# Kernel tuning notes

Measured on AMD Instinct MI355X. Metric: run time of the kernel, lower is better.

## Reference

```python
import jax, jax.numpy as jnp
import numpy as np
import math

B, S, D, H = 4, 1024, 2048, 16
DH = D // H          # dim_head = 128
DHID = 128           # dim_hid
DKER = 64            # dim_ker
EPS = 1e-6


def setup_inputs() -> dict:
    key = jax.random.key(0)
    ks = jax.random.split(key, 12)
    a1 = math.sqrt(6.0 / (DH + DHID))
    a2 = math.sqrt(6.0 / (DKER + DHID))
    a3 = math.sqrt(6.0 / (2 * DKER))
    return {
        "q": jax.random.normal(ks[0], (B, S, D), jnp.float32),
        "k": jax.random.normal(ks[1], (B, S, D), jnp.float32),
        "v": jax.random.normal(ks[2], (B, S, D), jnp.float32),
        "lr_attn_mask": jax.random.randint(ks[3], (B, 1, S, S), 0, 2).astype(bool),
        "sparse_norms_lse": jax.random.normal(ks[4], (B, H, S, 1), jnp.float32),
        "sparse_attn_weights": jax.random.normal(ks[5], (B, H, S, S), jnp.float32),
        "kernel_q_mat1": jax.random.uniform(ks[6], (H, DH, DHID), jnp.float32, -a1, a1),
        "kernel_k_mat1": jax.random.uniform(ks[7], (H, DH, DHID), jnp.float32, -a1, a1),
        "kernel_q_mat2": jax.random.uniform(ks[8], (H, DHID, DKER), jnp.float32, -a2, a2),
        "kernel_k_mat2": jax.random.uniform(ks[9], (H, DHID, DKER), jnp.float32, -a2, a2),
        "interaction_k": jax.random.uniform(ks[10], (H, DKER, DKER), jnp.float32, -a3, a3),
        "scalingD": jnp.ones((1, H, 1, DKER), jnp.float32) * 1e-4,
        "scalingD2": jnp.ones((1, H, 1, DKER), jnp.float32) * 1e-4,
        "lambda_constant": 1,
    }


def _gelu(x):
    # torch F.gelu default = exact (erf) gelu
    return jax.nn.gelu(x, approximate=False)


def reference(q, k, v, lr_attn_mask, sparse_norms_lse, sparse_attn_weights,
              kernel_q_mat1, kernel_k_mat1, kernel_q_mat2, kernel_k_mat2,
              interaction_k, scalingD, scalingD2, lambda_constant):
    # split heads: [B,S,D] -> [B,H,S,DH]
    qh = q.reshape(B, S, H, DH).transpose(0, 2, 1, 3)
    kh = k.reshape(B, S, H, DH).transpose(0, 2, 1, 3)
    vh = v.reshape(B, S, H, DH).transpose(0, 2, 1, 3)

    # learned kernel feature maps (dropout=0 -> identity)
    qf = _gelu(jnp.einsum('bhsd,hde->bhse', qh, kernel_q_mat1))
    qf = _gelu(jnp.einsum('bhse,hef->bhsf', qf, kernel_q_mat2))

    kf = _gelu(jnp.einsum('bhsd,hde->bhse', kh, kernel_k_mat1))
    kf = jnp.abs(scalingD) * _gelu(jnp.einsum('bhse,hef->bhsf', kf, kernel_k_mat2))
    kf = kf + jnp.einsum('bhse,hef->bhsf', kf, interaction_k) * scalingD2

    # low-rank (kernelized) scores, masked. [B,H,S,S]
    scores = jnp.einsum('bhse,bhte->bhst', jnp.abs(qf), jnp.abs(kf))
    m = lr_attn_mask.astype(scores.dtype)  # [B,1,S,S] broadcasts
    scores = m * scores

    # log-domain merge with external sparse attention
    lr_norms_lse = jnp.log(scores.sum(axis=-1, keepdims=True) + EPS)
    norm_factor_lse = jnp.logaddexp(lr_norms_lse, sparse_norms_lse)
    logits = jnp.log(scores + EPS) * m + (1.0 - m) * sparse_attn_weights
    attn = jnp.exp(logits - norm_factor_lse)

    out = jnp.einsum('bhst,bhtd->bhsd', attn, vh)
    return out.transpose(0, 2, 1, 3).reshape(B, S, D)
```

## Files before the change

### kernel.cpp

```cpp
#include <hip/hip_runtime.h>


typedef __bf16 bf16_t;
typedef __attribute__((ext_vector_type(8))) __bf16 bf16x8;
typedef __attribute__((ext_vector_type(4))) float f32x4;

#define MFMA(a, b, c) __builtin_amdgcn_mfma_f32_16x16x32_bf16((a), (b), (c), 0, 0, 0)

typedef __attribute__((address_space(3))) void as3_void;
typedef __attribute__((address_space(1))) const void as1_void;
static __device__ __forceinline__ void gload16(const void* g, void* l) {
    __builtin_amdgcn_global_load_lds((as1_void*)g, (as3_void*)l, 16, 0, 0);
}

static __device__ __forceinline__ float gelu_exact(float x) {
    return 0.5f * x * (1.0f + erff(x * 0.70710678118654752f));
}

__global__ __launch_bounds__(256) void conv_weights_kernel(
    const float* __restrict__ wq1, const float* __restrict__ wk1,
    const float* __restrict__ wq2, const float* __restrict__ wk2,
    const float* __restrict__ iK,
    bf16_t* __restrict__ wq1t, bf16_t* __restrict__ wk1t,
    bf16_t* __restrict__ wq2t, bf16_t* __restrict__ wk2t,
    bf16_t* __restrict__ iKt)
{
    const int idx = blockIdx.x * 256 + threadIdx.x;
    if (idx < 16 * 128 * 128) {
        int h = idx >> 14, e = (idx >> 7) & 127, d = idx & 127;
        wq1t[idx] = (bf16_t)wq1[(h << 14) + (d << 7) + e];
        wk1t[idx] = (bf16_t)wk1[(h << 14) + (d << 7) + e];
    }
    if (idx < 16 * 64 * 128) {
        int h = idx >> 13, f = (idx >> 7) & 63, e = idx & 127;
        wq2t[idx] = (bf16_t)wq2[(h << 13) + (e << 6) + f];
        wk2t[idx] = (bf16_t)wk2[(h << 13) + (e << 6) + f];
    }
    if (idx < 16 * 64 * 64) {
        int h = idx >> 12, g = (idx >> 6) & 63, f = idx & 63;
        iKt[idx] = (bf16_t)iK[(h << 12) + (f << 6) + g];
    }
}

__global__ __launch_bounds__(256) void conv_v_kernel(
    const float* __restrict__ v, bf16_t* __restrict__ vT)
{
    __shared__ bf16_t tr[128][72];
    const int bh = blockIdx.x, b = bh >> 4, h = bh & 15;
    const int tt = blockIdx.y;
    const int t0 = tt * 64;
    const int tid = threadIdx.x;
#pragma unroll
    for (int i = 0; i < 8; ++i) {
        int f4 = tid + 256 * i;
        int t = f4 >> 5, c4 = f4 & 31;
        const float4 vv = *reinterpret_cast<const float4*>(
            &v[((size_t)b * 1024 + t0 + t) * 2048 + h * 128 + c4 * 4]);
        tr[c4 * 4 + 0][t] = (bf16_t)vv.x;
        tr[c4 * 4 + 1][t] = (bf16_t)vv.y;
        tr[c4 * 4 + 2][t] = (bf16_t)vv.z;
        tr[c4 * 4 + 3][t] = (bf16_t)vv.w;
    }
    __syncthreads();
#pragma unroll
    for (int i = 0; i < 32; ++i) {
        int e = tid + 256 * i;
        int d = e >> 6, tl = e & 63;
        vT[(((size_t)bh * 16 + tt) * 128 + d) * 64 + tl] = tr[d][tl];
    }
}

__global__ __launch_bounds__(256) void feat_kernel(
    const float* __restrict__ q, const float* __restrict__ k,
    const bf16_t* __restrict__ wq1t, const bf16_t* __restrict__ wq2t,
    const bf16_t* __restrict__ wk1t, const bf16_t* __restrict__ wk2t,
    const bf16_t* __restrict__ iKt,
    const float* __restrict__ sD, const float* __restrict__ sD2,
    bf16_t* __restrict__ qf, bf16_t* __restrict__ kf)
{
    __shared__ bf16_t xa[64][136];
    __shared__ bf16_t h1[64][136];
    __shared__ bf16_t k2[64][72];

    const int tid = threadIdx.x;
    const int lane = tid & 63, w = tid >> 6;
    const int lr = lane & 15, lg = lane >> 4;
    const int row0 = blockIdx.x * 64;
    const int h = blockIdx.y;
    const int path = blockIdx.z;

    const float* X = path ? k : q;
    const bf16_t* w1t = path ? wk1t : wq1t;
    const bf16_t* w2t = path ? wk2t : wq2t;
    bf16_t* outp = path ? kf : qf;

#pragma unroll
    for (int i = 0; i < 8; ++i) {
        int f4 = tid + 256 * i;
        int r = f4 >> 5, c4 = f4 & 31;
        const float4 vv = *reinterpret_cast<const float4*>(
            &X[(size_t)(row0 + r) * 2048 + h * 128 + c4 * 4]);
        xa[r][c4 * 4 + 0] = (bf16_t)vv.x;
        xa[r][c4 * 4 + 1] = (bf16_t)vv.y;
        xa[r][c4 * 4 + 2] = (bf16_t)vv.z;
        xa[r][c4 * 4 + 3] = (bf16_t)vv.w;
    }
    __syncthreads();

    bf16x8 a1[4];
#pragma unroll
    for (int kk = 0; kk < 4; ++kk)
        a1[kk] = *reinterpret_cast<const bf16x8*>(&xa[w * 16 + lr][kk * 32 + lg * 8]);
#pragma unroll
    for (int nt = 0; nt < 8; ++nt) {
        f32x4 acc = {0.f, 0.f, 0.f, 0.f};
#pragma unroll
        for (int kk = 0; kk < 4; ++kk) {
            bf16x8 bfr = *reinterpret_cast<const bf16x8*>(
                &w1t[(size_t)h * 16384 + (nt * 16 + lr) * 128 + kk * 32 + lg * 8]);
            acc = MFMA(a1[kk], bfr, acc);
        }
#pragma unroll
        for (int r = 0; r < 4; ++r)
            h1[w * 16 + lg * 4 + r][nt * 16 + lr] = (bf16_t)gelu_exact(acc[r]);
    }
    __syncthreads();

    bf16x8 a2[4];
#pragma unroll
    for (int kk = 0; kk < 4; ++kk)
        a2[kk] = *reinterpret_cast<const bf16x8*>(&h1[w * 16 + lr][kk * 32 + lg * 8]);

    if (path == 0) {
#pragma unroll
        for (int nt = 0; nt < 4; ++nt) {
            f32x4 acc = {0.f, 0.f, 0.f, 0.f};
#pragma unroll
            for (int kk = 0; kk < 4; ++kk) {
                bf16x8 bfr = *reinterpret_cast<const bf16x8*>(
                    &w2t[(size_t)h * 8192 + (nt * 16 + lr) * 128 + kk * 32 + lg * 8]);
                acc = MFMA(a2[kk], bfr, acc);
            }
#pragma unroll
            for (int r = 0; r < 4; ++r) {
                int n = row0 + w * 16 + lg * 4 + r;
                int bb = n >> 10, s = n & 1023;
                outp[(((size_t)bb * 16 + h) * 1024 + s) * 64 + nt * 16 + lr] =
                    (bf16_t)fabsf(gelu_exact(acc[r]));
            }
        }
    } else {
#pragma unroll
        for (int nt = 0; nt < 4; ++nt) {
            f32x4 acc = {0.f, 0.f, 0.f, 0.f};
#pragma unroll
            for (int kk = 0; kk < 4; ++kk) {
                bf16x8 bfr = *reinterpret_cast<const bf16x8*>(
                    &w2t[(size_t)h * 8192 + (nt * 16 + lr) * 128 + kk * 32 + lg * 8]);
                acc = MFMA(a2[kk], bfr, acc);
            }
#pragma unroll
            for (int r = 0; r < 4; ++r) {
                int f = nt * 16 + lr;
                k2[w * 16 + lg * 4 + r][f] =
                    (bf16_t)(fabsf(sD[h * 64 + f]) * gelu_exact(acc[r]));
            }
        }
        __syncthreads();
        bf16x8 a3[2];
#pragma unroll
        for (int kk = 0; kk < 2; ++kk)
            a3[kk] = *reinterpret_cast<const bf16x8*>(&k2[w * 16 + lr][kk * 32 + lg * 8]);
#pragma unroll
        for (int nt = 0; nt < 4; ++nt) {
            f32x4 acc = {0.f, 0.f, 0.f, 0.f};
#pragma unroll
            for (int kk = 0; kk < 2; ++kk) {
                bf16x8 bfr = *reinterpret_cast<const bf16x8*>(
                    &iKt[(size_t)h * 4096 + (nt * 16 + lr) * 64 + kk * 32 + lg * 8]);
                acc = MFMA(a3[kk], bfr, acc);
            }
#pragma unroll
            for (int r = 0; r < 4; ++r) {
                int row = w * 16 + lg * 4 + r;
                int g = nt * 16 + lr;
                float base = (float)k2[row][g];
                float kv = fabsf(base + acc[r] * sD2[h * 64 + g]);
                int n = row0 + row;
                int bb = n >> 10, s = n & 1023;
                outp[(((size_t)bb * 16 + h) * 1024 + s) * 64 + g] = (bf16_t)kv;
            }
        }
    }
}

__global__ __launch_bounds__(256, 2) void attn_fused_kernel(
    const bf16_t* __restrict__ qf, const bf16_t* __restrict__ kf,
    const bf16_t* __restrict__ vT,
    const unsigned char* __restrict__ mask8,
    const float* __restrict__ saw, const float* __restrict__ lse,
    float* __restrict__ out)
{
    __shared__ bf16_t vbuf[2][128 * 64];
    __shared__ bf16_t ebuf[2][64 * 72];
    __shared__ int mflag;

    const int tid = threadIdx.x;
    const int lane = tid & 63, w = tid >> 6;
    const int lr = lane & 15, lg = lane >> 4;

    const int di = blockIdx.y * 16 + blockIdx.x;
    const int xcd = di & 7, rr = di >> 3;
    const int bh = xcd + 8 * (rr >> 4);
    const int s0 = (rr & 15) * 64;
    const int b = bh >> 4, h = bh & 15;

    if (tid == 0) {
        unsigned a = 0;
        for (int i = 0; i < 64; ++i) a |= mask8[4 * i + 1];
        mflag = (a == 0) ? 1 : 0;
    }
    __syncthreads();
    const bool mask_is_int = (mflag != 0);
    const int* mask32 = (const int*)mask8;

    const int strow = tid >> 4;
    const int stcol = (tid & 15) * 4;
    const size_t saw_base = ((size_t)bh << 20) + (size_t)(s0 + strow) * 1024 + stcol;
    const size_t m_base   = ((size_t)b << 20) + (size_t)(s0 + strow) * 1024 + stcol;

    const int vrow = tid >> 3;
    const int vcol8 = (tid & 7) ^ (vrow & 7);
    const bf16_t* vt_bh = vT + (size_t)bh * 131072;

    bf16x8 aq0, aq1;
    {
        const size_t qb = ((size_t)bh * 1024 + s0 + w * 16 + lr) * 64;
        aq0 = *reinterpret_cast<const bf16x8*>(&qf[qb + lg * 8]);
        aq1 = *reinterpret_cast<const bf16x8*>(&qf[qb + 32 + lg * 8]);
    }

    const f32x4 fzero = {0.f, 0.f, 0.f, 0.f};
    f32x4 oacc[8];
#pragma unroll
    for (int i = 0; i < 8; ++i) oacc[i] = fzero;
    float rowsum[4] = {0.f, 0.f, 0.f, 0.f};

#define STAGE_VT(BUF, TILE)                                                      \
    {                                                                            \
        const bf16_t* vg = vt_bh + (size_t)(TILE) * 8192 + vcol8 * 8;            \
        char* lb = (char*)&vbuf[BUF][0] + w * 1024;                              \
        _Pragma("unroll")                                                        \
        for (int j = 0; j < 4; ++j)                                              \
            gload16(vg + (size_t)(32 * j + vrow) * 64, lb + j * 4096);           \
    }

#define LOAD_KF(TILE, KR)                                                        \
    {                                                                            \
        _Pragma("unroll")                                                        \
        for (int nt = 0; nt < 4; ++nt) {                                         \
            const size_t kb = ((size_t)bh * 1024 + (TILE) * 64 + nt * 16 + lr) * 64; \
            KR[nt * 2]     = *reinterpret_cast<const bf16x8*>(&kf[kb + lg * 8]); \
            KR[nt * 2 + 1] = *reinterpret_cast<const bf16x8*>(&kf[kb + 32 + lg * 8]); \
        }                                                                        \
    }

#define LOAD_SAWM(TILE, SS, MI, MU)                                              \
    {                                                                            \
        _Pragma("unroll")                                                        \
        for (int j = 0; j < 4; ++j)                                              \
            SS[j] = *reinterpret_cast<const float4*>(                            \
                &saw[saw_base + (size_t)(TILE) * 64 + (size_t)j * 16384]);       \
        if (mask_is_int) {                                                       \
            _Pragma("unroll")                                                    \
            for (int j = 0; j < 4; ++j)                                          \
                MI[j] = *reinterpret_cast<const int4*>(                          \
                    &mask32[m_base + (size_t)(TILE) * 64 + (size_t)j * 16384]);  \
        } else {                                                                 \
            _Pragma("unroll")                                                    \
            for (int j = 0; j < 4; ++j)                                          \
                MU[j] = *reinterpret_cast<const unsigned*>(                      \
                    &mask8[m_base + (size_t)(TILE) * 64 + (size_t)j * 16384]);   \
        }                                                                        \
    }

#define WRITE_EBUF(BUF, SS, MI, MU)                                              \
    {                                                                            \
        _Pragma("unroll")                                                        \
        for (int j = 0; j < 4; ++j) {                                            \
            int m0, m1, m2, m3;                                                  \
            if (mask_is_int) {                                                   \
                m0 = MI[j].x; m1 = MI[j].y; m2 = MI[j].z; m3 = MI[j].w;          \
            } else {                                                             \
                m0 = (int)(MU[j] & 255u);        m1 = (int)((MU[j] >> 8) & 255u);\
                m2 = (int)((MU[j] >> 16) & 255u); m3 = (int)(MU[j] >> 24);       \
            }                                                                    \
            bf16_t e[4];                                                         \
            e[0] = m0 ? (bf16_t)(-1.0f) : (bf16_t)__expf(SS[j].x);               \
            e[1] = m1 ? (bf16_t)(-1.0f) : (bf16_t)__expf(SS[j].y);               \
            e[2] = m2 ? (bf16_t)(-1.0f) : (bf16_t)__expf(SS[j].z);               \
            e[3] = m3 ? (bf16_t)(-1.0f) : (bf16_t)__expf(SS[j].w);               \
            *reinterpret_cast<uint2*>(&ebuf[BUF][(strow + 16 * j) * 72 + stcol]) \
                = *reinterpret_cast<const uint2*>(e);                            \
        }                                                                        \
    }

#define PHASE(CUR, KR)                                                           \
    {                                                                            \
        f32x4 c[4];                                                              \
        _Pragma("unroll")                                                        \
        for (int nt = 0; nt < 4; ++nt) {                                         \
            f32x4 acc = fzero;                                                   \
            acc = MFMA(aq0, KR[nt * 2], acc);                                    \
            acc = MFMA(aq1, KR[nt * 2 + 1], acc);                                \
            c[nt] = acc;                                                         \
        }                                                                        \
        _Pragma("unroll")                                                        \
        for (int nt = 0; nt < 4; ++nt) {                                         \
            _Pragma("unroll")                                                    \
            for (int r = 0; r < 4; ++r) {                                        \
                const int eoff = (w * 16 + lg * 4 + r) * 72 + nt * 16 + lr;      \
                float pe = (float)ebuf[CUR][eoff];                               \
                float sc = c[nt][r];                                             \
                bool msk = pe < 0.f;                                             \
                float wv = msk ? (sc + 1e-6f) : pe;                              \
                rowsum[r] += msk ? sc : 0.f;                                     \
                ebuf[CUR][eoff] = (bf16_t)wv;                                    \
            }                                                                    \
        }                                                                        \
        asm volatile("s_waitcnt lgkmcnt(0)" ::: "memory");                       \
        __builtin_amdgcn_sched_barrier(0);                                       \
        bf16x8 ap0 = *reinterpret_cast<const bf16x8*>(                           \
            &ebuf[CUR][(w * 16 + lr) * 72 + lg * 8]);                            \
        bf16x8 ap1 = *reinterpret_cast<const bf16x8*>(                           \
            &ebuf[CUR][(w * 16 + lr) * 72 + 32 + lg * 8]);                       \
        const char* vb = (const char*)&vbuf[CUR][0];                             \
        _Pragma("unroll")                                                        \
        for (int dt = 0; dt < 8; ++dt) {                                         \
            const int row = dt * 16 + lr;                                        \
            bf16x8 v0 = *reinterpret_cast<const bf16x8*>(                        \
                vb + row * 128 + ((lg * 16) ^ xorv));                            \
            bf16x8 v1 = *reinterpret_cast<const bf16x8*>(                        \
                vb + row * 128 + ((64 + lg * 16) ^ xorv));                       \
            oacc[dt] = MFMA(ap0, v0, oacc[dt]);                                  \
            oacc[dt] = MFMA(ap1, v1, oacc[dt]);                                  \
        }                                                                        \
    }

    float4 sawA[4], sawB[4];
    int4 miA[4], miB[4];
    unsigned muA[4], muB[4];
    bf16x8 kfA[8], kfB[8];
    const int xorv = (lr & 7) << 4;

    LOAD_SAWM(0, sawA, miA, muA);
    WRITE_EBUF(0, sawA, miA, muA);
    LOAD_SAWM(1, sawA, miA, muA);
    LOAD_KF(0, kfA);
    STAGE_VT(0, 0);
    __syncthreads();

    for (int i = 0; i < 16; i += 2) {
        STAGE_VT(1, i + 1);
        LOAD_KF(i + 1, kfB);
        LOAD_SAWM((i + 2) & 15, sawB, miB, muB);
        PHASE(0, kfA);
        WRITE_EBUF(1, sawA, miA, muA);
        __syncthreads();
        STAGE_VT(0, (i + 2) & 15);
        LOAD_KF((i + 2) & 15, kfA);
        LOAD_SAWM((i + 3) & 15, sawA, miA, muA);
        PHASE(1, kfB);
        WRITE_EBUF(0, sawB, miB, muB);
        __syncthreads();
    }

#pragma unroll
    for (int r = 0; r < 4; ++r) {
        float s = rowsum[r];
#pragma unroll
        for (int m = 1; m < 16; m <<= 1) s += __shfl_xor(s, m);
        rowsum[r] = s;
    }
    float invden[4];
#pragma unroll
    for (int r = 0; r < 4; ++r) {
        const int srow = s0 + w * 16 + lg * 4 + r;
        invden[r] = 1.0f / (rowsum[r] + 1e-6f + __expf(lse[(size_t)bh * 1024 + srow]));
    }
#pragma unroll
    for (int dt = 0; dt < 8; ++dt) {
#pragma unroll
        for (int r = 0; r < 4; ++r) {
            const int srow = s0 + w * 16 + lg * 4 + r;
            out[((size_t)b * 1024 + srow) * 2048 + h * 128 + dt * 16 + lr] =
                oacc[dt][r] * invden[r];
        }
    }
#undef STAGE_VT
#undef LOAD_KF
#undef LOAD_SAWM
#undef WRITE_EBUF
#undef PHASE
}

extern "C" void kernel_launch(void* const* d_in, const int* in_sizes, int n_in,
                              void* d_out, int out_size, void* d_ws, size_t ws_size,
                              hipStream_t stream)
{
    const float* q   = (const float*)d_in[0];
    const float* k   = (const float*)d_in[1];
    const float* v   = (const float*)d_in[2];
    const unsigned char* mask = (const unsigned char*)d_in[3];
    const float* lse = (const float*)d_in[4];
    const float* saw = (const float*)d_in[5];
    const float* wq1 = (const float*)d_in[6];
    const float* wk1 = (const float*)d_in[7];
    const float* wq2 = (const float*)d_in[8];
    const float* wk2 = (const float*)d_in[9];
    const float* iK  = (const float*)d_in[10];
    const float* sD  = (const float*)d_in[11];
    const float* sD2 = (const float*)d_in[12];
    float* out = (float*)d_out;

    bf16_t* wsb  = (bf16_t*)d_ws;
    bf16_t* wq1t = wsb;
    bf16_t* wk1t = wq1t + 262144;
    bf16_t* wq2t = wk1t + 262144;
    bf16_t* wk2t = wq2t + 131072;
    bf16_t* iKt  = wk2t + 131072;
    bf16_t* qf   = iKt  + 65536;
    bf16_t* kf   = qf   + 4194304;
    bf16_t* vT   = kf   + 4194304;

    conv_weights_kernel<<<dim3(1024), dim3(256), 0, stream>>>(
        wq1, wk1, wq2, wk2, iK, wq1t, wk1t, wq2t, wk2t, iKt);
    conv_v_kernel<<<dim3(64, 16), dim3(256), 0, stream>>>(v, vT);
    feat_kernel<<<dim3(64, 16, 2), dim3(256), 0, stream>>>(
        q, k, wq1t, wq2t, wk1t, wk2t, iKt, sD, sD2, qf, kf);
    attn_fused_kernel<<<dim3(16, 64), dim3(256), 0, stream>>>(
        qf, kf, vT, mask, saw, lse, out);
}
```

Before: 212.1 us.

## Swap MFMA operand order in attention and pre-normalize mask into byte buffer

```diff
diff --git a/kernel.cpp b/kernel.cpp
--- a/kernel.cpp
+++ b/kernel.cpp
@@ -15,6 +15,13 @@
 
 static __device__ __forceinline__ float gelu_exact(float x) {
     return 0.5f * x * (1.0f + erff(x * 0.70710678118654752f));
+}
+
+static __device__ __forceinline__ unsigned pack_bf16(float a, float b) {
+    bf16_t x = (bf16_t)a, y = (bf16_t)b;
+    unsigned short ux = __builtin_bit_cast(unsigned short, x);
+    unsigned short uy = __builtin_bit_cast(unsigned short, y);
+    return (unsigned)ux | ((unsigned)uy << 16);
 }
 
 __global__ __launch_bounds__(256) void conv_weights_kernel(
@@ -39,6 +46,47 @@
     if (idx < 16 * 64 * 64) {
         int h = idx >> 12, g = (idx >> 6) & 63, f = idx & 63;
         iKt[idx] = (bf16_t)iK[(h << 12) + (f << 6) + g];
+    }
+}
+
+__global__ __launch_bounds__(256) void prep_mask_kernel(
+    const unsigned char* __restrict__ mask8, unsigned char* __restrict__ mout)
+{
+    __shared__ int mflag;
+    const int tid = threadIdx.x;
+    if (tid == 0) {
+        unsigned a = 0;
+        for (int i = 0; i < 64; ++i) a |= mask8[4 * i + 1];
+        mflag = (a == 0) ? 1 : 0;
+    }
+    __syncthreads();
+    const size_t base = ((size_t)blockIdx.x * 256 + tid) * 16;
+    if (mflag) {
+        const int* mi = (const int*)mask8;
+        uint4 r;
+        unsigned bs[4];
+#pragma unroll
+        for (int j = 0; j < 4; ++j) {
+            int4 v = *reinterpret_cast<const int4*>(&mi[base + j * 4]);
+            bs[j] = (v.x ? 1u : 0u) | ((v.y ? 1u : 0u) << 8) |
+                    ((v.z ? 1u : 0u) << 16) | ((v.w ? 1u : 0u) << 24);
+        }
+        r.x = bs[0]; r.y = bs[1]; r.z = bs[2]; r.w = bs[3];
+        *reinterpret_cast<uint4*>(&mout[base]) = r;
+    } else {
+        uint4 v = *reinterpret_cast<const uint4*>(&mask8[base]);
+        uint4 r;
+        unsigned* pv = (unsigned*)&v;
+        unsigned* pr = (unsigned*)&r;
+#pragma unroll
+        for (int j = 0; j < 4; ++j) {
+            unsigned x = pv[j], o = 0;
+#pragma unroll
+            for (int k = 0; k < 4; ++k)
+                o |= (((x >> (8 * k)) & 255u) ? 1u : 0u) << (8 * k);
+            pr[j] = o;
+        }
+        *reinterpret_cast<uint4*>(&mout[base]) = r;
     }
 }
 
@@ -194,16 +242,15 @@
     }
 }
 
-__global__ __launch_bounds__(256, 2) void attn_fused_kernel(
+__global__ __launch_bounds__(256, 3) void attn_swapped_kernel(
     const bf16_t* __restrict__ qf, const bf16_t* __restrict__ kf,
     const bf16_t* __restrict__ vT,
-    const unsigned char* __restrict__ mask8,
+    const unsigned char* __restrict__ mprep,
     const float* __restrict__ saw, const float* __restrict__ lse,
     float* __restrict__ out)
 {
     __shared__ bf16_t vbuf[2][128 * 64];
-    __shared__ bf16_t ebuf[2][64 * 72];
-    __shared__ int mflag;
+    __shared__ unsigned p_lds[4][16][36];
 
     const int tid = threadIdx.x;
     const int lane = tid & 63, w = tid >> 6;
@@ -215,19 +262,9 @@
     const int s0 = (rr & 15) * 64;
     const int b = bh >> 4, h = bh & 15;
 
-    if (tid == 0) {
-        unsigned a = 0;
-        for (int i = 0; i < 64; ++i) a |= mask8[4 * i + 1];
-        mflag = (a == 0) ? 1 : 0;
-    }
-    __syncthreads();
-    const bool mask_is_int = (mflag != 0);
-    const int* mask32 = (const int*)mask8;
-
-    const int strow = tid >> 4;
-    const int stcol = (tid & 15) * 4;
-    const size_t saw_base = ((size_t)bh << 20) + (size_t)(s0 + strow) * 1024 + stcol;
-    const size_t m_base   = ((size_t)b << 20) + (size_t)(s0 + strow) * 1024 + stcol;
+    const int srow = s0 + w * 16 + lr;
+    const size_t saw_row = ((size_t)bh << 20) + (size_t)srow * 1024;
+    const size_t m_row   = ((size_t)b << 20) + (size_t)srow * 1024;
 
     const int vrow = tid >> 3;
     const int vcol8 = (tid & 7) ^ (vrow & 7);
@@ -235,7 +272,7 @@
 
     bf16x8 aq0, aq1;
     {
-        const size_t qb = ((size_t)bh * 1024 + s0 + w * 16 + lr) * 64;
+        const size_t qb = ((size_t)bh * 1024 + srow) * 64;
         aq0 = *reinterpret_cast<const bf16x8*>(&qf[qb + lg * 8]);
         aq1 = *reinterpret_cast<const bf16x8*>(&qf[qb + 32 + lg * 8]);
     }
@@ -244,7 +281,8 @@
     f32x4 oacc[8];
 #pragma unroll
     for (int i = 0; i < 8; ++i) oacc[i] = fzero;
-    float rowsum[4] = {0.f, 0.f, 0.f, 0.f};
+    float rowsum = 0.f;
+    const int xorv = (lr & 7) << 4;
 
 #define STAGE_VT(BUF, TILE)                                                      \
     {                                                                            \
@@ -255,6 +293,17 @@
             gload16(vg + (size_t)(32 * j + vrow) * 64, lb + j * 4096);           \
     }
 
+#define LOAD_SAW(TILE, SS, MM)                                                   \
+    {                                                                            \
+        _Pragma("unroll")                                                        \
+        for (int nt = 0; nt < 4; ++nt) {                                         \
+            SS[nt] = *reinterpret_cast<const f32x4*>(                            \
+                &saw[saw_row + (TILE) * 64 + nt * 16 + lg * 4]);                 \
+            MM[nt] = *reinterpret_cast<const unsigned*>(                         \
+                &mprep[m_row + (TILE) * 64 + nt * 16 + lg * 4]);                 \
+        }                                                                        \
+    }
+
 #define LOAD_KF(TILE, KR)                                                        \
     {                                                                            \
         _Pragma("unroll")                                                        \
@@ -265,75 +314,55 @@
         }                                                                        \
     }
 
-#define LOAD_SAWM(TILE, SS, MI, MU)                                              \
-    {                                                                            \
-        _Pragma("unroll")                                                        \
-        for (int j = 0; j < 4; ++j)                                              \
-            SS[j] = *reinterpret_cast<const float4*>(                            \
-                &saw[saw_base + (size_t)(TILE) * 64 + (size_t)j * 16384]);       \
-        if (mask_is_int) {                                                       \
-            _Pragma("unroll")                                                    \
-            for (int j = 0; j < 4; ++j)                                          \
-                MI[j] = *reinterpret_cast<const int4*>(                          \
-                    &mask32[m_base + (size_t)(TILE) * 64 + (size_t)j * 16384]);  \
-        } else {                                                                 \
-            _Pragma("unroll")                                                    \
-            for (int j = 0; j < 4; ++j)                                          \
-                MU[j] = *reinterpret_cast<const unsigned*>(                      \
-                    &mask8[m_base + (size_t)(TILE) * 64 + (size_t)j * 16384]);   \
-        }                                                                        \
-    }
-
-#define WRITE_EBUF(BUF, SS, MI, MU)                                              \
-    {                                                                            \
-        _Pragma("unroll")                                                        \
-        for (int j = 0; j < 4; ++j) {                                            \
-            int m0, m1, m2, m3;                                                  \
-            if (mask_is_int) {                                                   \
-                m0 = MI[j].x; m1 = MI[j].y; m2 = MI[j].z; m3 = MI[j].w;          \
-            } else {                                                             \
-                m0 = (int)(MU[j] & 255u);        m1 = (int)((MU[j] >> 8) & 255u);\
-                m2 = (int)((MU[j] >> 16) & 255u); m3 = (int)(MU[j] >> 24);       \
-            }                                                                    \
-            bf16_t e[4];                                                         \
-            e[0] = m0 ? (bf16_t)(-1.0f) : (bf16_t)__expf(SS[j].x);               \
-            e[1] = m1 ? (bf16_t)(-1.0f) : (bf16_t)__expf(SS[j].y);               \
-            e[2] = m2 ? (bf16_t)(-1.0f) : (bf16_t)__expf(SS[j].z);               \
-            e[3] = m3 ? (bf16_t)(-1.0f) : (bf16_t)__expf(SS[j].w);               \
-            *reinterpret_cast<uint2*>(&ebuf[BUF][(strow + 16 * j) * 72 + stcol]) \
-                = *reinterpret_cast<const uint2*>(e);                            \
-        }                                                                        \
-    }
-
-#define PHASE(CUR, KR)                                                           \
+#define PHASE(CUR, SS, MM)                                                       \
     {                                                                            \
         f32x4 c[4];                                                              \
         _Pragma("unroll")                                                        \
         for (int nt = 0; nt < 4; ++nt) {                                         \
             f32x4 acc = fzero;                                                   \
-            acc = MFMA(aq0, KR[nt * 2], acc);                                    \
-            acc = MFMA(aq1, KR[nt * 2 + 1], acc);                                \
+            acc = MFMA(kfR[nt * 2], aq0, acc);                                   \
+            acc = MFMA(kfR[nt * 2 + 1], aq1, acc);                               \
             c[nt] = acc;                                                         \
         }                                                                        \
+        unsigned pk[8];                                                          \
         _Pragma("unroll")                                                        \
         for (int nt = 0; nt < 4; ++nt) {                                         \
-            _Pragma("unroll")                                                    \
-            for (int r = 0; r < 4; ++r) {                                        \
-                const int eoff = (w * 16 + lg * 4 + r) * 72 + nt * 16 + lr;      \
-                float pe = (float)ebuf[CUR][eoff];                               \
-                float sc = c[nt][r];                                             \
-                bool msk = pe < 0.f;                                             \
-                float wv = msk ? (sc + 1e-6f) : pe;                              \
-                rowsum[r] += msk ? sc : 0.f;                                     \
-                ebuf[CUR][eoff] = (bf16_t)wv;                                    \
+            float v0, v1, v2, v3;                                                \
+            {                                                                    \
+                unsigned m0 = (MM[nt]) & 255u;                                   \
+                float sc = c[nt][0];                                             \
+                v0 = m0 ? (sc + 1e-6f) : __expf(SS[nt][0]);                      \
+                rowsum += m0 ? sc : 0.f;                                         \
             }                                                                    \
-        }                                                                        \
-        asm volatile("s_waitcnt lgkmcnt(0)" ::: "memory");                       \
-        __builtin_amdgcn_sched_barrier(0);                                       \
-        bf16x8 ap0 = *reinterpret_cast<const bf16x8*>(                           \
-            &ebuf[CUR][(w * 16 + lr) * 72 + lg * 8]);                            \
-        bf16x8 ap1 = *reinterpret_cast<const bf16x8*>(                           \
-            &ebuf[CUR][(w * 16 + lr) * 72 + 32 + lg * 8]);                       \
+            {                                                                    \
+                unsigned m1 = (MM[nt] >> 8) & 255u;                              \
+                float sc = c[nt][1];                                             \
+                v1 = m1 ? (sc + 1e-6f) : __expf(SS[nt][1]);                      \
+                rowsum += m1 ? sc : 0.f;                                         \
+            }                                                                    \
+            {                                                                    \
+                unsigned m2 = (MM[nt] >> 16) & 255u;                             \
+                float sc = c[nt][2];                                             \
+                v2 = m2 ? (sc + 1e-6f) : __expf(SS[nt][2]);                      \
+                rowsum += m2 ? sc : 0.f;                                         \
+            }                                                                    \
+            {                                                                    \
+                unsigned m3 = (MM[nt] >> 24) & 255u;                             \
+                float sc = c[nt][3];                                             \
+                v3 = m3 ? (sc + 1e-6f) : __expf(SS[nt][3]);                      \
+                rowsum += m3 ? sc : 0.f;                                         \
+            }                                                                    \
+            pk[nt * 2]     = pack_bf16(v0, v1);                                  \
+            pk[nt * 2 + 1] = pack_bf16(v2, v3);                                  \
+        }                                                                        \
+                  \
+        _Pragma("unroll")                                                        \
+        for (int nt = 0; nt < 4; ++nt) {                                         \
+            uint2 wv; wv.x = pk[nt * 2]; wv.y = pk[nt * 2 + 1];                  \
+            *reinterpret_cast<uint2*>(&p_lds[w][lr][nt * 8 + lg * 2]) = wv;      \
+        }                                                                        \
+        bf16x8 pb0 = *reinterpret_cast<const bf16x8*>(&p_lds[w][lr][lg * 4]);    \
+        bf16x8 pb1 = *reinterpret_cast<const bf16x8*>(&p_lds[w][lr][16 + lg * 4]); \
         const char* vb = (const char*)&vbuf[CUR][0];                             \
         _Pragma("unroll")                                                        \
         for (int dt = 0; dt < 8; ++dt) {                                         \
@@ -342,65 +371,50 @@
                 vb + row * 128 + ((lg * 16) ^ xorv));                            \
             bf16x8 v1 = *reinterpret_cast<const bf16x8*>(                        \
                 vb + row * 128 + ((64 + lg * 16) ^ xorv));                       \
-            oacc[dt] = MFMA(ap0, v0, oacc[dt]);                                  \
-            oacc[dt] = MFMA(ap1, v1, oacc[dt]);                                  \
-        }                                                                        \
-    }
-
-    float4 sawA[4], sawB[4];
-    int4 miA[4], miB[4];
+            oacc[dt] = MFMA(v0, pb0, oacc[dt]);                                  \
+            oacc[dt] = MFMA(v1, pb1, oacc[dt]);                                  \
+        }                                                                        \
+    }
+
+    f32x4 sawA[4], sawB[4];
     unsigned muA[4], muB[4];
-    bf16x8 kfA[8], kfB[8];
-    const int xorv = (lr & 7) << 4;
-
-    LOAD_SAWM(0, sawA, miA, muA);
-    WRITE_EBUF(0, sawA, miA, muA);
-    LOAD_SAWM(1, sawA, miA, muA);
-    LOAD_KF(0, kfA);
+    bf16x8 kfR[8];
+
+    LOAD_SAW(0, sawA, muA);
     STAGE_VT(0, 0);
     __syncthreads();
 
     for (int i = 0; i < 16; i += 2) {
         STAGE_VT(1, i + 1);
-        LOAD_KF(i + 1, kfB);
-        LOAD_SAWM((i + 2) & 15, sawB, miB, muB);
-        PHASE(0, kfA);
-        WRITE_EBUF(1, sawA, miA, muA);
+        LOAD_SAW(i + 1, sawB, muB);
+        LOAD_KF(i, kfR);
+        PHASE(0, sawA, muA);
         __syncthreads();
         STAGE_VT(0, (i + 2) & 15);
-        LOAD_KF((i + 2) & 15, kfA);
-        LOAD_SAWM((i + 3) & 15, sawA, miA, muA);
-        PHASE(1, kfB);
-        WRITE_EBUF(0, sawB, miB, muB);
+        LOAD_SAW((i + 2) & 15, sawA, muA);
+        LOAD_KF(i + 1, kfR);
+        PHASE(1, sawB, muB);
         __syncthreads();
     }
 
-#pragma unroll
-    for (int r = 0; r < 4; ++r) {
-        float s = rowsum[r];
-#pragma unroll
-        for (int m = 1; m < 16; m <<= 1) s += __shfl_xor(s, m);
-        rowsum[r] = s;
-    }
-    float invden[4];
-#pragma unroll
-    for (int r = 0; r < 4; ++r) {
-        const int srow = s0 + w * 16 + lg * 4 + r;
-        invden[r] = 1.0f / (rowsum[r] + 1e-6f + __expf(lse[(size_t)bh * 1024 + srow]));
-    }
+    rowsum += __shfl_xor(rowsum, 16);
+    rowsum += __shfl_xor(rowsum, 32);
+    const float invden =
+        1.0f / (rowsum + 1e-6f + __expf(lse[(size_t)bh * 1024 + srow]));
+
+    const size_t ob = ((size_t)b * 1024 + srow) * 2048 + h * 128 + lg * 4;
 #pragma unroll
     for (int dt = 0; dt < 8; ++dt) {
-#pragma unroll
-        for (int r = 0; r < 4; ++r) {
-            const int srow = s0 + w * 16 + lg * 4 + r;
-            out[((size_t)b * 1024 + srow) * 2048 + h * 128 + dt * 16 + lr] =
-                oacc[dt][r] * invden[r];
-        }
+        f32x4 o;
+        o[0] = oacc[dt][0] * invden;
+        o[1] = oacc[dt][1] * invden;
+        o[2] = oacc[dt][2] * invden;
+        o[3] = oacc[dt][3] * invden;
+        *reinterpret_cast<f32x4*>(&out[ob + dt * 16]) = o;
     }
 #undef STAGE_VT
+#undef LOAD_SAW
 #undef LOAD_KF
-#undef LOAD_SAWM
-#undef WRITE_EBUF
 #undef PHASE
 }
 
@@ -432,12 +446,14 @@
     bf16_t* qf   = iKt  + 65536;
     bf16_t* kf   = qf   + 4194304;
     bf16_t* vT   = kf   + 4194304;
+    unsigned char* mprep = (unsigned char*)(vT + 8388608);
 
     conv_weights_kernel<<<dim3(1024), dim3(256), 0, stream>>>(
         wq1, wk1, wq2, wk2, iK, wq1t, wk1t, wq2t, wk2t, iKt);
+    prep_mask_kernel<<<dim3(1024), dim3(256), 0, stream>>>(mask, mprep);
     conv_v_kernel<<<dim3(64, 16), dim3(256), 0, stream>>>(v, vT);
     feat_kernel<<<dim3(64, 16, 2), dim3(256), 0, stream>>>(
         q, k, wq1t, wq2t, wk1t, wk2t, iKt, sD, sD2, qf, kf);
-    attn_fused_kernel<<<dim3(16, 64), dim3(256), 0, stream>>>(
-        qf, kf, vT, mask, saw, lse, out);
-}
+    attn_swapped_kernel<<<dim3(16, 64), dim3(256), 0, stream>>>(
+        qf, kf, vT, mprep, saw, lse, out);
+}
```

Result: slower. 250.8 us (+18.2%).
